# Kernel tuning notes

Measured on AMD Instinct MI355X. Metric: run time of the kernel, lower is better.

The kernel has to match this reference:

```python
import jax, jax.numpy as jnp
import numpy as np

MAX_VIEWS = 50   # n_view in _hard_anchor_sampling
IGNORE = 255
TEMP = 0.07


def _sample_indices(labels, predict, max_classes, n_view, rng):
    # Faithful numpy port of _hard_anchor_sampling's index selection
    # (hard = predicted-as-c but mislabeled, easy = correct), host-side since
    # the torch original is data-dependent (nonzero/randperm per class).
    B, N = labels.shape
    idx = np.zeros((B, max_classes, n_view), dtype=np.int64)
    half = n_view // 2
    for b in range(B):
        yh, y = labels[b], predict[b]
        cls = [c for c in np.unique(yh) if c != IGNORE and (yh == c).sum() > n_view]
        for n, c in enumerate(cls[:max_classes]):
            hard = np.where((yh == c) & (y != c))[0]
            easy = np.where((yh == c) & (y == c))[0]
            nh_, ne_ = len(hard), len(easy)
            if nh_ >= half and ne_ >= half:
                nh, ne = half, n_view - half
            elif nh_ >= half:
                ne = ne_; nh = n_view - ne
            else:
                nh = nh_; ne = n_view - nh
            sel = np.concatenate([rng.permutation(hard)[:nh], rng.permutation(easy)[:ne]])
            idx[b, n] = sel
        # with uniform random labels over 19 classes and 16384 pixels, every
        # class qualifies, so the 'fill remaining slots' branch never triggers.
    return idx


def setup_inputs() -> dict:
    B, C, H, W = 4, 256, 128, 128
    NC = 19
    key = jax.random.key(0)
    k1, k2 = jax.random.split(key)
    feats_q = jax.random.normal(k1, (B, C, H, W), dtype=jnp.float32)
    feats_k = jax.random.normal(k2, (B, C, H, W), dtype=jnp.float32)
    rng = np.random.default_rng(0)
    labels = rng.integers(0, NC, size=(B, H * W))
    predict = rng.integers(0, NC, size=(B, H * W))
    sample_idx = jnp.asarray(_sample_indices(labels, predict, NC, MAX_VIEWS, rng))
    return {"feats_q": feats_q, "feats_k": feats_k, "sample_idx": sample_idx}


def _neg_cols(nc, nv):
    # static column indices surviving the ~diag_block boolean mask (row-major)
    P = nc * nv
    cols = np.arange(P)
    return np.stack([cols[(cols // nv) != (i // nv)] for i in range(P)])  # [P, P-nv]


def _forward(feats_q, feats_k, sample_idx):
    B, C, H, W = feats_q.shape
    _, nc, nv = sample_idx.shape
    P = nc * nv
    q = feats_q.transpose(0, 2, 3, 1).reshape(B, H * W, C)
    k = jax.lax.stop_gradient(feats_k).transpose(0, 2, 3, 1).reshape(B, H * W, C)  # detach
    bidx = jnp.arange(B)[:, None, None]
    Xq = q[bidx, sample_idx]  # [B, nc, nv, C] gathered anchors
    Xk = k[bidx, sample_idx]
    # positives: per-patch q.k
    l_pos = jnp.einsum('bnvc,bnvc->bnv', Xq, Xk).reshape(-1, 1)  # [B*P, 1]
    # negatives: full within-batch similarity, minus same-class diagonal blocks
    qf = Xq.reshape(B, P, C)
    kf = Xk.reshape(B, P, C)
    sim = jnp.einsum('bpc,bqc->bpq', qf, kf)  # [B, P, P]
    neg_cols = jnp.asarray(_neg_cols(nc, nv))  # [P, P-nv]
    l_neg = jnp.take_along_axis(sim, neg_cols[None], axis=2).reshape(B * P, P - nv)
    out = jnp.concatenate([l_pos, l_neg], axis=1) / TEMP
    # CrossEntropyLoss(reduction='none') with target 0
    return -jax.nn.log_softmax(out, axis=1)[:, 0]  # [B*P]


def reference(feats_q, feats_k, sample_idx):
    return _forward(feats_q, feats_k, sample_idx)
```

## Files before the change

### kernel.cpp

```cpp
#include <hip/hip_runtime.h>
#include <math.h>

#define BB 4
#define CC 256
#define HW (128*128)
#define NC 19
#define NV 50
#define PP 950
#define INV_T (1.0f/0.07f)
#define PLANE ((size_t)BB * PP * CC)
#define NCG 8
#define LDSP 40

typedef short bf16x8 __attribute__((ext_vector_type(8)));
typedef float f32x4  __attribute__((ext_vector_type(4)));

static __device__ __forceinline__ unsigned short f2bf(float f) {
    unsigned int u = __float_as_uint(f);
    unsigned int r = (u + 0x7fffu + ((u >> 16) & 1u)) >> 16;
    return (unsigned short)r;
}
static __device__ __forceinline__ float bf2f(unsigned short h) {
    return __uint_as_float(((unsigned int)h) << 16);
}
__device__ __forceinline__ void lse_merge(float& m, float& s, float m2, float s2) {
    float nm = fmaxf(m, m2);
    float e1 = __expf(m - nm);
    float e2 = __expf(m2 - nm);
    s = s * e1 + s2 * e2;
    m = nm;
}

__global__ __launch_bounds__(1024)
void mapbuild_kernel(const int* __restrict__ sidx, short* __restrict__ map) {
    int b = blockIdx.x;
    int tid = threadIdx.x;
    int4* m4 = (int4*)(map + (size_t)b * HW);
    int4 mone = make_int4(-1, -1, -1, -1);
    m4[tid] = mone;
    m4[tid + 1024] = mone;
    __syncthreads();
    if (tid < PP) {
        int pix = sidx[b * PP + tid];
        map[(size_t)b * HW + pix] = (short)tid;
    }
}

__global__ __launch_bounds__(256)
void gather_kernel(const float* __restrict__ fq, const float* __restrict__ fk,
                   const short* __restrict__ map,
                   unsigned short* __restrict__ xqh, unsigned short* __restrict__ xql,
                   unsigned short* __restrict__ xkh, unsigned short* __restrict__ xkl) {
    int x = blockIdx.x;
    int chunk  = x & 63;
    int cg     = (x >> 6) & 7;
    int tensor = (x >> 9) & 1;
    int b      = x >> 10;
    int px0 = chunk * 256;

    __shared__ short mp[256];
    int tid = threadIdx.x;
    if (tid < 32)
        ((int4*)mp)[tid] = ((const int4*)(map + (size_t)b * HW + px0))[tid];
    __syncthreads();

    const float* f = tensor ? fk : fq;
    unsigned short* oh = tensor ? xkh : xqh;
    unsigned short* ol = tensor ? xkl : xql;

    int lp  = tid & 15;
    int chl = tid >> 4;
    int ch0 = cg * 32 + chl;
    int ch1 = ch0 + 16;
    const float* s0 = f + ((size_t)b * CC + ch0) * HW + px0;
    const float* s1 = f + ((size_t)b * CC + ch1) * HW + px0;

    float4 v[8];
#pragma unroll
    for (int i = 0; i < 4; ++i) v[i]     = *(const float4*)(s0 + (i * 16 + lp) * 4);
#pragma unroll
    for (int i = 0; i < 4; ++i) v[4 + i] = *(const float4*)(s1 + (i * 16 + lp) * 4);

#pragma unroll
    for (int k = 0; k < 8; ++k) {
        int i  = k & 3;
        int ch = (k < 4) ? ch0 : ch1;
#pragma unroll
        for (int e = 0; e < 4; ++e) {
            int px = (i * 16 + lp) * 4 + e;
            int slot = mp[px];
            if (slot >= 0) {
                float val = ((const float*)&v[k])[e];
                unsigned short h = f2bf(val);
                size_t dst = ((size_t)b * PP + slot) * CC + ch;
                oh[dst] = h;
                ol[dst] = f2bf(val - bf2f(h));
            }
        }
    }
}

#define MF(ACC, AF, BF) ACC = __builtin_amdgcn_mfma_f32_16x16x32_bf16(AF, BF, ACC, 0, 0, 0)

#define STEP(KT) do {                                                           \
    int4 rh_, rl_;                                                              \
    if ((KT) < 7) {                                                             \
        rh_ = *(const int4*)(xkh + stage_src + ((KT) + 1) * 32);                \
        rl_ = *(const int4*)(xkl + stage_src + ((KT) + 1) * 32);                \
    }                                                                           \
    const short* bbase_ = &bl[(KT) & 1][0][0] + lr * LDSP + lg * 8;             \
    _Pragma("unroll")                                                           \
    for (int ct = 0; ct < 8; ++ct) {                                            \
        const short* bp_ = bbase_ + ct * (16 * LDSP);                           \
        bf16x8 Bh_ = *(const bf16x8*)bp_;                                       \
        bf16x8 Bl_ = *(const bf16x8*)(bp_ + 128 * LDSP);                        \
        MF(acc[ct], Ah[KT], Bh_);                                               \
        MF(acc[ct], Al[KT], Bh_);                                               \
        MF(acc[ct], Ah[KT], Bl_);                                               \
    }                                                                           \
    if ((KT) < 7) {                                                             \
        *(int4*)&bl[((KT) + 1) & 1][0][stage_dst] = rh_;                        \
        *(int4*)&bl[((KT) + 1) & 1][1][stage_dst] = rl_;                        \
        __syncthreads();                                                        \
    }                                                                           \
} while (0)

__global__ __launch_bounds__(512)
void nce_mfma(const unsigned short* __restrict__ xqh, const unsigned short* __restrict__ xql,
              const unsigned short* __restrict__ xkh, const unsigned short* __restrict__ xkl,
              float* __restrict__ pos, float* __restrict__ pm, float* __restrict__ ps) {
    __shared__ short bl[2][2][128 * LDSP];

    int cg = blockIdx.x;
    int rb = blockIdx.y;
    int b  = blockIdx.z;
    int tid = threadIdx.x;
    int w = tid >> 6, l = tid & 63;
    int lr = l & 15, lg = l >> 4;

    int uc = tid >> 2, uq = tid & 3;
    int gcol = cg * 128 + uc; if (gcol > PP - 1) gcol = PP - 1;
    size_t stage_src = ((size_t)b * PP + gcol) * CC + uq * 8;
    int stage_dst = uc * LDSP + uq * 8;

    int arow = rb * 128 + w * 16 + lr; if (arow > PP - 1) arow = PP - 1;
    size_t abase = ((size_t)b * PP + arow) * CC + lg * 8;
    bf16x8 Ah[8], Al[8];
#pragma unroll
    for (int kt = 0; kt < 8; ++kt) {
        Ah[kt] = *(const bf16x8*)(xqh + abase + kt * 32);
        Al[kt] = *(const bf16x8*)(xql + abase + kt * 32);
    }

    {
        int4 rh = *(const int4*)(xkh + stage_src);
        int4 rl = *(const int4*)(xkl + stage_src);
        *(int4*)&bl[0][0][stage_dst] = rh;
        *(int4*)&bl[0][1][stage_dst] = rl;
    }
    __syncthreads();

    f32x4 acc[8];
#pragma unroll
    for (int ct = 0; ct < 8; ++ct) acc[ct] = (f32x4){0.f, 0.f, 0.f, 0.f};

    STEP(0); STEP(1); STEP(2); STEP(3);
    STEP(4); STEP(5); STEP(6); STEP(7);

#pragma unroll
    for (int j = 0; j < 4; ++j) {
        int row = rb * 128 + w * 16 + lg * 4 + j;
        bool rowok = row < PP;
        int rcls = row / NV;
        float m = -1e30f, s = 0.f;
#pragma unroll
        for (int ct = 0; ct < 8; ++ct) {
            int col = cg * 128 + ct * 16 + lr;
            bool colok = col < PP;
            int ccls = col / NV;
            float x = acc[ct][j] * INV_T;
            bool ok = rowok && colok && ((ccls != rcls) || (col == row));
            if (rowok && col == row) pos[(size_t)b * 960 + row] = x;
            float xm = ok ? x : -1e30f;
            float nm = fmaxf(m, xm);
            float e1 = __expf(m - nm);
            float e2 = ok ? __expf(x - nm) : 0.f;
            s = s * e1 + e2; m = nm;
        }
#pragma unroll
        for (int off = 1; off <= 8; off <<= 1) {
            float m2 = __shfl_xor(m, off, 64);
            float s2 = __shfl_xor(s, off, 64);
            lse_merge(m, s, m2, s2);
        }
        if (lr == 0 && rowok) {
            pm[((size_t)b * NCG + cg) * 960 + row] = m;
            ps[((size_t)b * NCG + cg) * 960 + row] = s;
        }
    }
}

__global__ __launch_bounds__(256)
void finalize_kernel(const float* __restrict__ pm, const float* __restrict__ ps,
                     const float* __restrict__ pos, float* __restrict__ out) {
    int i = blockIdx.x * 256 + threadIdx.x;
    if (i >= BB * PP) return;
    int b = i / PP, row = i - b * PP;
    float m = -1e30f, s = 0.f;
#pragma unroll
    for (int g = 0; g < NCG; ++g) {
        size_t o = ((size_t)b * NCG + g) * 960 + row;
        lse_merge(m, s, pm[o], ps[o]);
    }
    out[i] = m + logf(s) - pos[(size_t)b * 960 + row];
}

extern "C" void kernel_launch(void* const* d_in, const int* in_sizes, int n_in,
                              void* d_out, int out_size, void* d_ws, size_t ws_size,
                              hipStream_t stream) {
    const float* fq   = (const float*)d_in[0];
    const float* fk   = (const float*)d_in[1];
    const int*   sidx = (const int*)d_in[2];
    float* outp = (float*)d_out;

    char* p = (char*)d_ws;
    unsigned short* xqh = (unsigned short*)p; p += PLANE * 2;
    unsigned short* xql = (unsigned short*)p; p += PLANE * 2;
    unsigned short* xkh = (unsigned short*)p; p += PLANE * 2;
    unsigned short* xkl = (unsigned short*)p; p += PLANE * 2;
    short*          map = (short*)p;          p += (size_t)BB * HW * 2;
    float*          pos = (float*)p;          p += (size_t)BB * 960 * 4;
    float*           pm = (float*)p;          p += (size_t)BB * NCG * 960 * 4;
    float*           ps = (float*)p;

    mapbuild_kernel<<<dim3(BB), 1024, 0, stream>>>(sidx, map);
    gather_kernel<<<dim3(4096), 256, 0, stream>>>(fq, fk, map, xqh, xql, xkh, xkl);
    nce_mfma<<<dim3(NCG, 8, BB), 512, 0, stream>>>(xqh, xql, xkh, xkl, pos, pm, ps);
    finalize_kernel<<<dim3((BB * PP + 255) / 256), 256, 0, stream>>>(pm, ps, pos, outp);
}
```

Measured before the change: 52.37 us.

## Stage gathered features in LDS and write coalesced 16-byte rows per chunk

The pixel-to-slot map is replaced by per-chunk compact lists of sampled pixels, built with shared-memory atomics. The gather kernel now stages the bf16 hi/lo values in LDS and writes each sampled row's 32-channel slice as 16-byte vector stores, instead of scattering 2-byte stores with stride CC. The block index order is also permuted so the channel group is the slowest dimension. The cost is an extra LDS round trip and a synchronization. Entries beyond 64 per 256-pixel chunk are dropped, which would silently lose samples if any chunk overflowed.

Result: no change. 51.47 us (-1.7%).

```diff
diff --git a/kernel.cpp b/kernel.cpp
--- a/kernel.cpp
+++ b/kernel.cpp
@@ -11,6 +11,8 @@
 #define PLANE ((size_t)BB * PP * CC)
 #define NCG 8
 #define LDSP 40
+#define NCHK 64
+#define MAXE 64
 
 typedef short bf16x8 __attribute__((ext_vector_type(8)));
 typedef float f32x4  __attribute__((ext_vector_type(4)));
@@ -32,36 +34,56 @@
 }
 
 __global__ __launch_bounds__(1024)
-void mapbuild_kernel(const int* __restrict__ sidx, short* __restrict__ map) {
+void mapbuild_kernel(const int* __restrict__ sidx,
+                     int* __restrict__ clist, int* __restrict__ ccnt) {
+    __shared__ int lcnt[NCHK];
+    __shared__ int lent[NCHK * MAXE];
     int b = blockIdx.x;
     int tid = threadIdx.x;
-    int4* m4 = (int4*)(map + (size_t)b * HW);
-    int4 mone = make_int4(-1, -1, -1, -1);
-    m4[tid] = mone;
-    m4[tid + 1024] = mone;
+    if (tid < NCHK) lcnt[tid] = 0;
     __syncthreads();
     if (tid < PP) {
         int pix = sidx[b * PP + tid];
-        map[(size_t)b * HW + pix] = (short)tid;
-    }
+        int chunk = pix >> 8, pl = pix & 255;
+        int pos = atomicAdd(&lcnt[chunk], 1);
+        if (pos < MAXE) lent[chunk * MAXE + pos] = (tid << 8) | pl;
+    }
+    __syncthreads();
+    if (tid < NCHK) {
+        int c = lcnt[tid];
+        ccnt[b * NCHK + tid] = c < MAXE ? c : MAXE;
+    }
+    for (int i = tid; i < NCHK * MAXE; i += 1024)
+        clist[b * NCHK * MAXE + i] = lent[i];
 }
 
 __global__ __launch_bounds__(256)
 void gather_kernel(const float* __restrict__ fq, const float* __restrict__ fk,
-                   const short* __restrict__ map,
+                   const int* __restrict__ clist, const int* __restrict__ ccnt,
                    unsigned short* __restrict__ xqh, unsigned short* __restrict__ xql,
                    unsigned short* __restrict__ xkh, unsigned short* __restrict__ xkl) {
+    __shared__ short pxmap[256];
+    __shared__ short slotarr[MAXE];
+    __shared__ short bufh[MAXE][32];
+    __shared__ short bufl[MAXE][32];
+
     int x = blockIdx.x;
     int chunk  = x & 63;
-    int cg     = (x >> 6) & 7;
-    int tensor = (x >> 9) & 1;
-    int b      = x >> 10;
+    int tensor = (x >> 6) & 1;
+    int b      = (x >> 7) & 3;
+    int cg     = x >> 9;
     int px0 = chunk * 256;
 
-    __shared__ short mp[256];
     int tid = threadIdx.x;
-    if (tid < 32)
-        ((int4*)mp)[tid] = ((const int4*)(map + (size_t)b * HW + px0))[tid];
+    int cnt = ccnt[b * NCHK + chunk];
+
+    pxmap[tid] = -1;
+    __syncthreads();
+    if (tid < cnt) {
+        int e = clist[(b * NCHK + chunk) * MAXE + tid];
+        slotarr[tid] = (short)(e >> 8);
+        pxmap[e & 255] = (short)tid;
+    }
     __syncthreads();
 
     const float* f = tensor ? fk : fq;
@@ -83,19 +105,31 @@
 
 #pragma unroll
     for (int k = 0; k < 8; ++k) {
-        int i  = k & 3;
-        int ch = (k < 4) ? ch0 : ch1;
+        int i = k & 3;
+        int lch = (k < 4) ? chl : (chl + 16);
 #pragma unroll
         for (int e = 0; e < 4; ++e) {
-            int px = (i * 16 + lp) * 4 + e;
-            int slot = mp[px];
-            if (slot >= 0) {
+            int px = i * 64 + lp * 4 + e;
+            int le = pxmap[px];
+            if (le >= 0) {
                 float val = ((const float*)&v[k])[e];
                 unsigned short h = f2bf(val);
-                size_t dst = ((size_t)b * PP + slot) * CC + ch;
-                oh[dst] = h;
-                ol[dst] = f2bf(val - bf2f(h));
+                bufh[le][lch] = (short)h;
+                bufl[le][lch] = (short)f2bf(val - bf2f(h));
             }
+        }
+    }
+    __syncthreads();
+
+#pragma unroll
+    for (int rep = 0; rep < 2; ++rep) {
+        int e = rep * 32 + (tid >> 3);
+        int plane = (tid >> 2) & 1, q = tid & 3;
+        if (e < cnt) {
+            int slot = slotarr[e];
+            size_t dst = ((size_t)b * PP + slot) * CC + cg * 32 + q * 8;
+            const short* sp = (plane ? &bufl[e][0] : &bufh[e][0]) + q * 8;
+            *(int4*)((plane ? ol : oh) + dst) = *(const int4*)sp;
         }
     }
 }
@@ -228,13 +262,14 @@
     unsigned short* xql = (unsigned short*)p; p += PLANE * 2;
     unsigned short* xkh = (unsigned short*)p; p += PLANE * 2;
     unsigned short* xkl = (unsigned short*)p; p += PLANE * 2;
-    short*          map = (short*)p;          p += (size_t)BB * HW * 2;
+    int*          clist = (int*)p;            p += (size_t)BB * NCHK * MAXE * 4;
+    int*           ccnt = (int*)p;            p += (size_t)BB * NCHK * 4;
     float*          pos = (float*)p;          p += (size_t)BB * 960 * 4;
     float*           pm = (float*)p;          p += (size_t)BB * NCG * 960 * 4;
     float*           ps = (float*)p;
 
-    mapbuild_kernel<<<dim3(BB), 1024, 0, stream>>>(sidx, map);
-    gather_kernel<<<dim3(4096), 256, 0, stream>>>(fq, fk, map, xqh, xql, xkh, xkl);
+    mapbuild_kernel<<<dim3(BB), 1024, 0, stream>>>(sidx, clist, ccnt);
+    gather_kernel<<<dim3(4096), 256, 0, stream>>>(fq, fk, clist, ccnt, xqh, xql, xkh, xkl);
     nce_mfma<<<dim3(NCG, 8, BB), 512, 0, stream>>>(xqh, xql, xkh, xkl, pos, pm, ps);
     finalize_kernel<<<dim3((BB * PP + 255) / 256), 256, 0, stream>>>(pm, ps, pos, outp);
 }
```
